# Kernel tuning notes

Hardware: AMD Instinct MI355X
Metric: run time of the kernel (lower is better)

The kernel has to match this reference:

```python
import jax, jax.numpy as jnp
import numpy as np

NCLS, NDF, B = 256, 512, 1024
ALP = 0.1


def setup_inputs() -> dict:
    key = jax.random.key(0)
    k1, k2, k3 = jax.random.split(key, 3)
    df = jax.random.normal(k1, (B, NDF), dtype=jnp.float32)
    gt = jax.random.randint(k2, (B,), 0, NCLS)
    fc = jax.random.normal(k3, (NCLS, NDF), dtype=jnp.float32)
    return {"df": df, "gt": gt, "fc": fc}


def _update_stats(df, gt):
    """Sequential per-sample running mean/var update (moving_avg=False branch).
    Faithful to the torch no_grad loop: per-class counter `it`, c1=it/(it+1),
    c2=1/(it+1); mean[t]=f when it==0 else mean[t]*c1+f*c2;
    var[t]=var[t]*c1 + (f-mean[t])**2 * c1*c2. Buffers start at zero.
    """
    mean0 = jnp.zeros((NCLS, NDF), jnp.float32)
    var0 = jnp.zeros((NCLS, NDF), jnp.float32)
    it0 = jnp.zeros((NCLS,), jnp.int32)

    def step(carry, xt):
        mean, var, it = carry
        f, t = xt
        n = it[t]
        nf = n.astype(jnp.float32)
        c1 = nf / (nf + 1.0)
        c2 = 1.0 / (nf + 1.0)
        m_t = jnp.where(n == 0, f, mean[t] * c1 + f * c2)
        a = (f - m_t) ** 2
        v_t = var[t] * c1 + a * c1 * c2
        return (mean.at[t].set(m_t), var.at[t].set(v_t), it.at[t].add(1)), None

    (mean, var, it), _ = jax.lax.scan(step, (mean0, var0, it0), (df, gt))
    return mean, var


def reference(df, gt, fc):
    # stats updated from detached features (torch uses no_grad)
    _, var = _update_stats(jax.lax.stop_gradient(df), gt)
    Var = var[gt]          # (B, ndf)
    Fc = fc[gt]            # (B, ndf): column of fc for each sample's class
    W = fc[None, :, :] - Fc[:, None, :]  # (B, ncls, ndf)
    # score[b,c] = W[b,c,:].df[b,:] + alp/2 * (W**2)[b,c,:].Var[b,:]
    score = jnp.einsum('bcd,bd->bc', W, df) \
        + 0.5 * ALP * jnp.einsum('bcd,bd->bc', W * W, Var)
    return score[:, :, None]  # (B, ncls, 1), matching torch matmul output
```

## Files before the change

### kernel.cpp

```cpp
#include <hip/hip_runtime.h>

#define NCLS 256
#define NDF  512
#define BSZ  1024
#define ALP  0.1f


typedef __attribute__((ext_vector_type(8))) short bf16x8;
typedef __attribute__((ext_vector_type(4))) float f32x4;

__device__ __forceinline__ unsigned rne_pk(float lo, float hi) {
    union { float f; unsigned u; } a, b;
    a.f = lo; b.f = hi;
    unsigned ua = (a.u + 0x7FFFu + ((a.u >> 16) & 1u)) >> 16;
    unsigned ub = (b.u + 0x7FFFu + ((b.u >> 16) & 1u)) & 0xFFFF0000u;
    return ua | ub;
}
__device__ __forceinline__ uint4 pk16(float4 p, float4 q) {
    uint4 r;
    r.x = rne_pk(p.x, p.y); r.y = rne_pk(p.z, p.w);
    r.z = rne_pk(q.x, q.y); r.w = rne_pk(q.z, q.w);
    return r;
}

__global__ __launch_bounds__(256) void fused_main(const float* __restrict__ df,
                                                  const int* __restrict__ gt,
                                                  const float* __restrict__ fc,
                                                  float* __restrict__ s1p,
                                                  float* __restrict__ Rp) {
    __shared__ union {
        struct { alignas(16) char A[64 * 256]; alignas(16) char B[64 * 256]; } g;
        struct { int gts[BSZ]; unsigned long long bmap[64 * 16]; } r;
    } sm;

    const int tid = threadIdx.x;
    const int bid = blockIdx.x;
    const int lane = tid & 63;
    const int wv = tid >> 6;
    const int wm = (wv >> 1) * 32, wn = (wv & 1) * 32;
    const int fr = lane & 15;
    const int fkb = (lane >> 4) * 16;
    const int fswz = (fr & 7) << 4;

    const int sr = tid >> 2;
    const int sswz = (sr & 7) << 4;
    char* arow = sm.g.A + sr * 256;
    char* brow = sm.g.B + sr * 256;

    f32x4 acc[2][2];
    acc[0][0] = 0.f; acc[0][1] = 0.f; acc[1][0] = 0.f; acc[1][1] = 0.f;

    auto mma_step = [&](int k0b) {
        const int kb = (k0b + fkb) ^ fswz;
        const bf16x8 aF0 = *(const bf16x8*)(sm.g.A + (wm + fr) * 256 + kb);
        const bf16x8 aF1 = *(const bf16x8*)(sm.g.A + (wm + 16 + fr) * 256 + kb);
        const bf16x8 bF0 = *(const bf16x8*)(sm.g.B + (wn + fr) * 256 + kb);
        const bf16x8 bF1 = *(const bf16x8*)(sm.g.B + (wn + 16 + fr) * 256 + kb);
        acc[0][0] = __builtin_amdgcn_mfma_f32_16x16x32_bf16(aF0, bF0, acc[0][0], 0, 0, 0);
        acc[0][1] = __builtin_amdgcn_mfma_f32_16x16x32_bf16(aF0, bF1, acc[0][1], 0, 0, 0);
        acc[1][0] = __builtin_amdgcn_mfma_f32_16x16x32_bf16(aF1, bF0, acc[1][0], 0, 0, 0);
        acc[1][1] = __builtin_amdgcn_mfma_f32_16x16x32_bf16(aF1, bF1, acc[1][1], 0, 0, 0);
    };
    auto store_tile = [&](float* base) {
#pragma unroll
        for (int mi = 0; mi < 2; ++mi)
#pragma unroll
            for (int ni = 0; ni < 2; ++ni)
#pragma unroll
                for (int r2 = 0; r2 < 4; ++r2)
                    base[(wm + mi * 16 + (lane >> 4) * 4 + r2) * NCLS + wn + ni * 16 + fr] =
                        acc[mi][ni][r2];
    };

    if (bid >= 128) {
        const int sid = bid - 128;
        const int z = sid & 3;
        const int tile = sid >> 2;
        const int bm = tile & 15, bn = tile >> 4;
        const float* Ag = df + (bm * 64 + sr) * NDF + z * 128 + (tid & 3) * 32;
        const float* Bg = fc + (bn * 64 + sr) * NDF + z * 128 + (tid & 3) * 32;
        const int kbase = (tid & 3) * 64;

        float4 a[8], b[8];
#pragma unroll
        for (int i = 0; i < 8; ++i) a[i] = ((const float4*)Ag)[i];
#pragma unroll
        for (int i = 0; i < 8; ++i) b[i] = ((const float4*)Bg)[i];
        *(uint4*)(arow + ((kbase + 0) ^ sswz)) = pk16(a[0], a[1]);
        *(uint4*)(arow + ((kbase + 16) ^ sswz)) = pk16(a[2], a[3]);
        *(uint4*)(arow + ((kbase + 32) ^ sswz)) = pk16(a[4], a[5]);
        *(uint4*)(arow + ((kbase + 48) ^ sswz)) = pk16(a[6], a[7]);
        *(uint4*)(brow + ((kbase + 0) ^ sswz)) = pk16(b[0], b[1]);
        *(uint4*)(brow + ((kbase + 16) ^ sswz)) = pk16(b[2], b[3]);
        *(uint4*)(brow + ((kbase + 32) ^ sswz)) = pk16(b[4], b[5]);
        *(uint4*)(brow + ((kbase + 48) ^ sswz)) = pk16(b[6], b[7]);
        __syncthreads();
        mma_step(0); mma_step(64); mma_step(128); mma_step(192);
        store_tile(s1p + z * (BSZ * NCLS) + (bm * 64) * NCLS + bn * 64);
    } else {
        const int z = bid & 7;
        const int tile = bid >> 3;
        const int bm = tile & 3, bn = tile >> 2;
        const int D0 = z * 64;
        const int clocal = sr;
        const int myclass = bm * 64 + clocal;
        const int dim0 = D0 + (tid & 3) * 16;
        const int kbl = (tid & 3) * 32;
        const int kbq = 128 + kbl;

        const float* Bg = fc + (bn * 64 + sr) * NDF + dim0;
        const float4 b0 = ((const float4*)Bg)[0], b1 = ((const float4*)Bg)[1],
                     b2 = ((const float4*)Bg)[2], b3 = ((const float4*)Bg)[3];

        for (int i = tid; i < BSZ; i += 256) sm.r.gts[i] = gt[i];
        for (int i = tid; i < 1024; i += 256) sm.r.bmap[i] = 0ull;
        __syncthreads();
        for (int i = tid; i < BSZ; i += 256) {
            const int c = sm.r.gts[i] - bm * 64;
            if ((unsigned)c < 64u) atomicOr(&sm.r.bmap[c * 16 + (i >> 6)], 1ull << (i & 63));
        }
        const float* fct = fc + myclass * NDF + dim0;
        float fcq[16];
        {
            const float4 q0 = ((const float4*)fct)[0], q1 = ((const float4*)fct)[1];
            const float4 q2 = ((const float4*)fct)[2], q3 = ((const float4*)fct)[3];
            fcq[0]=q0.x; fcq[1]=q0.y; fcq[2]=q0.z; fcq[3]=q0.w;
            fcq[4]=q1.x; fcq[5]=q1.y; fcq[6]=q1.z; fcq[7]=q1.w;
            fcq[8]=q2.x; fcq[9]=q2.y; fcq[10]=q2.z; fcq[11]=q2.w;
            fcq[12]=q3.x; fcq[13]=q3.y; fcq[14]=q3.z; fcq[15]=q3.w;
        }
        __syncthreads();

        float m[16], v[16];
#pragma unroll
        for (int j = 0; j < 16; ++j) { m[j] = 0.f; v[j] = 0.f; }
        float nf = 0.f;
        {
            int w = 0;
            unsigned long long bits = sm.r.bmap[clocal * 16];
            auto next = [&]() -> int {
                while (bits == 0ull) {
                    if (w >= 15) return -1;
                    bits = sm.r.bmap[clocal * 16 + (++w)];
                }
                const int b = __ffsll((unsigned long long)bits) - 1;
                bits &= bits - 1ull;
                return (w << 6) + b;
            };
            int cur = next();
            float f[16];
            if (cur >= 0) {
                const float* p = df + cur * NDF + dim0;
                const float4 q0 = ((const float4*)p)[0], q1 = ((const float4*)p)[1];
                const float4 q2 = ((const float4*)p)[2], q3 = ((const float4*)p)[3];
                f[0]=q0.x; f[1]=q0.y; f[2]=q0.z; f[3]=q0.w;
                f[4]=q1.x; f[5]=q1.y; f[6]=q1.z; f[7]=q1.w;
                f[8]=q2.x; f[9]=q2.y; f[10]=q2.z; f[11]=q2.w;
                f[12]=q3.x; f[13]=q3.y; f[14]=q3.z; f[15]=q3.w;
            }
            while (cur >= 0) {
                const int nxt = next();
                float g[16];
                if (nxt >= 0) {
                    const float* p = df + nxt * NDF + dim0;
                    const float4 q0 = ((const float4*)p)[0], q1 = ((const float4*)p)[1];
                    const float4 q2 = ((const float4*)p)[2], q3 = ((const float4*)p)[3];
                    g[0]=q0.x; g[1]=q0.y; g[2]=q0.z; g[3]=q0.w;
                    g[4]=q1.x; g[5]=q1.y; g[6]=q1.z; g[7]=q1.w;
                    g[8]=q2.x; g[9]=q2.y; g[10]=q2.z; g[11]=q2.w;
                    g[12]=q3.x; g[13]=q3.y; g[14]=q3.z; g[15]=q3.w;
                }
                const float c2 = 1.0f / (nf + 1.0f);
                const float c1 = nf * c2;
                const float c12 = c1 * c2;
#pragma unroll
                for (int j = 0; j < 16; ++j) {
                    m[j] = m[j] * c1 + f[j] * c2;
                    const float a = f[j] - m[j];
                    v[j] = v[j] * c1 + a * a * c12;
                }
                nf += 1.0f;
#pragma unroll
                for (int j = 0; j < 16; ++j) f[j] = g[j];
                cur = nxt;
            }
        }
        __syncthreads();

        {
            float4 l0, l1, l2, l3;
            l0.x=-2.f*fcq[0]*v[0];  l0.y=-2.f*fcq[1]*v[1];  l0.z=-2.f*fcq[2]*v[2];  l0.w=-2.f*fcq[3]*v[3];
            l1.x=-2.f*fcq[4]*v[4];  l1.y=-2.f*fcq[5]*v[5];  l1.z=-2.f*fcq[6]*v[6];  l1.w=-2.f*fcq[7]*v[7];
            l2.x=-2.f*fcq[8]*v[8];  l2.y=-2.f*fcq[9]*v[9];  l2.z=-2.f*fcq[10]*v[10]; l2.w=-2.f*fcq[11]*v[11];
            l3.x=-2.f*fcq[12]*v[12]; l3.y=-2.f*fcq[13]*v[13]; l3.z=-2.f*fcq[14]*v[14]; l3.w=-2.f*fcq[15]*v[15];
            float4 p0, p1, p2, p3;
            p0.x=v[0];  p0.y=v[1];  p0.z=v[2];  p0.w=v[3];
            p1.x=v[4];  p1.y=v[5];  p1.z=v[6];  p1.w=v[7];
            p2.x=v[8];  p2.y=v[9];  p2.z=v[10]; p2.w=v[11];
            p3.x=v[12]; p3.y=v[13]; p3.z=v[14]; p3.w=v[15];
            float4 s0, s1, s2, s3;
            s0.x=b0.x*b0.x; s0.y=b0.y*b0.y; s0.z=b0.z*b0.z; s0.w=b0.w*b0.w;
            s1.x=b1.x*b1.x; s1.y=b1.y*b1.y; s1.z=b1.z*b1.z; s1.w=b1.w*b1.w;
            s2.x=b2.x*b2.x; s2.y=b2.y*b2.y; s2.z=b2.z*b2.z; s2.w=b2.w*b2.w;
            s3.x=b3.x*b3.x; s3.y=b3.y*b3.y; s3.z=b3.z*b3.z; s3.w=b3.w*b3.w;
            *(uint4*)(arow + ((kbl + 0) ^ sswz)) = pk16(l0, l1);
            *(uint4*)(arow + ((kbl + 16) ^ sswz)) = pk16(l2, l3);
            *(uint4*)(arow + ((kbq + 0) ^ sswz)) = pk16(p0, p1);
            *(uint4*)(arow + ((kbq + 16) ^ sswz)) = pk16(p2, p3);
            *(uint4*)(brow + ((kbl + 0) ^ sswz)) = pk16(b0, b1);
            *(uint4*)(brow + ((kbl + 16) ^ sswz)) = pk16(b2, b3);
            *(uint4*)(brow + ((kbq + 0) ^ sswz)) = pk16(s0, s1);
            *(uint4*)(brow + ((kbq + 16) ^ sswz)) = pk16(s2, s3);
        }
        __syncthreads();
        mma_step(0); mma_step(64); mma_step(128); mma_step(192);
        store_tile(Rp + z * (NCLS * NCLS) + (bm * 64) * NCLS + bn * 64);
    }
}

__global__ __launch_bounds__(256) void epilogue_kernel(const float* __restrict__ s1p,
                                                       const float* __restrict__ Rp,
                                                       const int* __restrict__ gt,
                                                       float* __restrict__ out) {
    const int b = blockIdx.x * 4 + (threadIdx.x >> 6);
    const int cq = (threadIdx.x & 63) * 4;
    const int t = gt[b];
    float4 v1 = make_float4(0.f, 0.f, 0.f, 0.f);
    float v1t = 0.f;
#pragma unroll
    for (int zz = 0; zz < 4; ++zz) {
        const float* row = s1p + zz * (BSZ * NCLS) + b * NCLS;
        const float4 q = *(const float4*)(row + cq);
        v1.x += q.x; v1.y += q.y; v1.z += q.z; v1.w += q.w;
        v1t += row[t];
    }
    float4 vR = make_float4(0.f, 0.f, 0.f, 0.f);
    float vRt = 0.f;
#pragma unroll
    for (int zz = 0; zz < 8; ++zz) {
        const float* row = Rp + zz * (NCLS * NCLS) + t * NCLS;
        const float4 q = *(const float4*)(row + cq);
        vR.x += q.x; vR.y += q.y; vR.z += q.z; vR.w += q.w;
        vRt += row[t];
    }
    float4 o;
    o.x = (v1.x - v1t) + 0.5f * ALP * (vR.x - vRt);
    o.y = (v1.y - v1t) + 0.5f * ALP * (vR.y - vRt);
    o.z = (v1.z - v1t) + 0.5f * ALP * (vR.z - vRt);
    o.w = (v1.w - v1t) + 0.5f * ALP * (vR.w - vRt);
    *(float4*)(out + b * NCLS + cq) = o;
}

extern "C" void kernel_launch(void* const* d_in, const int* in_sizes, int n_in,
                              void* d_out, int out_size, void* d_ws, size_t ws_size,
                              hipStream_t stream) {
    const float* df = (const float*)d_in[0];
    const int* gt = (const int*)d_in[1];
    const float* fc = (const float*)d_in[2];
    float* out = (float*)d_out;

    float* ws = (float*)d_ws;
    float* s1p = ws;
    float* Rp = s1p + 4 * BSZ * NCLS;

    fused_main<<<384, 256, 0, stream>>>(df, gt, fc, s1p, Rp);
    epilogue_kernel<<<256, 256, 0, stream>>>(s1p, Rp, gt, out);
}
```

Before: 25.92 us.

## Move df·fc GEMM into epilogue kernel and precompute per-sample bias

The split-K df·fc^T GEMM that wrote four partial score slabs to workspace is removed from the first kernel. The second kernel now does the full-K GEMM on 32x32 tiles and applies the variance-term epilogue directly. The self-class term df·fc[gt] becomes a separate per-sample bias, computed by spare blocks of the first kernel with matching bf16 rounding. This drops the large s1p write and re-read in exchange for a longer K loop per block in the second kernel.

```diff
diff --git a/kernel.cpp b/kernel.cpp
--- a/kernel.cpp
+++ b/kernel.cpp
@@ -22,12 +22,17 @@
     r.z = rne_pk(q.x, q.y); r.w = rne_pk(q.z, q.w);
     return r;
 }
-
-__global__ __launch_bounds__(256) void fused_main(const float* __restrict__ df,
-                                                  const int* __restrict__ gt,
-                                                  const float* __restrict__ fc,
-                                                  float* __restrict__ s1p,
-                                                  float* __restrict__ Rp) {
+__device__ __forceinline__ float bf16r(float x) {
+    union { float f; unsigned u; } c; c.f = x;
+    c.u = (c.u + 0x7FFFu + ((c.u >> 16) & 1u)) & 0xFFFF0000u;
+    return c.f;
+}
+
+__global__ __launch_bounds__(256) void k1_R_bias(const float* __restrict__ df,
+                                                 const int* __restrict__ gt,
+                                                 const float* __restrict__ fc,
+                                                 float* __restrict__ Rp,
+                                                 float* __restrict__ bias1) {
     __shared__ union {
         struct { alignas(16) char A[64 * 256]; alignas(16) char B[64 * 256]; } g;
         struct { int gts[BSZ]; unsigned long long bmap[64 * 16]; } r;
@@ -36,6 +41,25 @@
     const int tid = threadIdx.x;
     const int bid = blockIdx.x;
     const int lane = tid & 63;
+
+    if (bid >= 128) {
+        const int b = (bid - 128) * 4 + (tid >> 6);
+        const int t = gt[b];
+        const float* pd = df + b * NDF + lane * 8;
+        const float* pf = fc + t * NDF + lane * 8;
+        const float4 d0 = ((const float4*)pd)[0], d1 = ((const float4*)pd)[1];
+        const float4 f0 = ((const float4*)pf)[0], f1 = ((const float4*)pf)[1];
+        float s = 0.f;
+        s = fmaf(bf16r(d0.x), bf16r(f0.x), s); s = fmaf(bf16r(d0.y), bf16r(f0.y), s);
+        s = fmaf(bf16r(d0.z), bf16r(f0.z), s); s = fmaf(bf16r(d0.w), bf16r(f0.w), s);
+        s = fmaf(bf16r(d1.x), bf16r(f1.x), s); s = fmaf(bf16r(d1.y), bf16r(f1.y), s);
+        s = fmaf(bf16r(d1.z), bf16r(f1.z), s); s = fmaf(bf16r(d1.w), bf16r(f1.w), s);
+#pragma unroll
+        for (int off = 32; off; off >>= 1) s += __shfl_xor(s, off, 64);
+        if (lane == 0) bias1[b] = s;
+        return;
+    }
+
     const int wv = tid >> 6;
     const int wm = (wv >> 1) * 32, wn = (wv & 1) * 32;
     const int fr = lane & 15;
@@ -61,194 +85,200 @@
         acc[1][0] = __builtin_amdgcn_mfma_f32_16x16x32_bf16(aF1, bF0, acc[1][0], 0, 0, 0);
         acc[1][1] = __builtin_amdgcn_mfma_f32_16x16x32_bf16(aF1, bF1, acc[1][1], 0, 0, 0);
     };
-    auto store_tile = [&](float* base) {
-#pragma unroll
-        for (int mi = 0; mi < 2; ++mi)
-#pragma unroll
-            for (int ni = 0; ni < 2; ++ni)
-#pragma unroll
-                for (int r2 = 0; r2 < 4; ++r2)
-                    base[(wm + mi * 16 + (lane >> 4) * 4 + r2) * NCLS + wn + ni * 16 + fr] =
-                        acc[mi][ni][r2];
-    };
-
-    if (bid >= 128) {
-        const int sid = bid - 128;
-        const int z = sid & 3;
-        const int tile = sid >> 2;
-        const int bm = tile & 15, bn = tile >> 4;
-        const float* Ag = df + (bm * 64 + sr) * NDF + z * 128 + (tid & 3) * 32;
-        const float* Bg = fc + (bn * 64 + sr) * NDF + z * 128 + (tid & 3) * 32;
-        const int kbase = (tid & 3) * 64;
-
-        float4 a[8], b[8];
-#pragma unroll
-        for (int i = 0; i < 8; ++i) a[i] = ((const float4*)Ag)[i];
-#pragma unroll
-        for (int i = 0; i < 8; ++i) b[i] = ((const float4*)Bg)[i];
-        *(uint4*)(arow + ((kbase + 0) ^ sswz)) = pk16(a[0], a[1]);
-        *(uint4*)(arow + ((kbase + 16) ^ sswz)) = pk16(a[2], a[3]);
-        *(uint4*)(arow + ((kbase + 32) ^ sswz)) = pk16(a[4], a[5]);
-        *(uint4*)(arow + ((kbase + 48) ^ sswz)) = pk16(a[6], a[7]);
-        *(uint4*)(brow + ((kbase + 0) ^ sswz)) = pk16(b[0], b[1]);
-        *(uint4*)(brow + ((kbase + 16) ^ sswz)) = pk16(b[2], b[3]);
-        *(uint4*)(brow + ((kbase + 32) ^ sswz)) = pk16(b[4], b[5]);
-        *(uint4*)(brow + ((kbase + 48) ^ sswz)) = pk16(b[6], b[7]);
-        __syncthreads();
-        mma_step(0); mma_step(64); mma_step(128); mma_step(192);
-        store_tile(s1p + z * (BSZ * NCLS) + (bm * 64) * NCLS + bn * 64);
-    } else {
-        const int z = bid & 7;
-        const int tile = bid >> 3;
-        const int bm = tile & 3, bn = tile >> 2;
-        const int D0 = z * 64;
-        const int clocal = sr;
-        const int myclass = bm * 64 + clocal;
-        const int dim0 = D0 + (tid & 3) * 16;
-        const int kbl = (tid & 3) * 32;
-        const int kbq = 128 + kbl;
-
-        const float* Bg = fc + (bn * 64 + sr) * NDF + dim0;
-        const float4 b0 = ((const float4*)Bg)[0], b1 = ((const float4*)Bg)[1],
-                     b2 = ((const float4*)Bg)[2], b3 = ((const float4*)Bg)[3];
-
-        for (int i = tid; i < BSZ; i += 256) sm.r.gts[i] = gt[i];
-        for (int i = tid; i < 1024; i += 256) sm.r.bmap[i] = 0ull;
-        __syncthreads();
-        for (int i = tid; i < BSZ; i += 256) {
-            const int c = sm.r.gts[i] - bm * 64;
-            if ((unsigned)c < 64u) atomicOr(&sm.r.bmap[c * 16 + (i >> 6)], 1ull << (i & 63));
+
+    const int z = bid & 7;
+    const int tile = bid >> 3;
+    const int bm = tile & 3, bn = tile >> 2;
+    const int D0 = z * 64;
+    const int clocal = sr;
+    const int myclass = bm * 64 + clocal;
+    const int dim0 = D0 + (tid & 3) * 16;
+    const int kbl = (tid & 3) * 32;
+    const int kbq = 128 + kbl;
+
+    const float* Bg = fc + (bn * 64 + sr) * NDF + dim0;
+    const float4 b0 = ((const float4*)Bg)[0], b1 = ((const float4*)Bg)[1],
+                 b2 = ((const float4*)Bg)[2], b3 = ((const float4*)Bg)[3];
+
+    for (int i = tid; i < BSZ; i += 256) sm.r.gts[i] = gt[i];
+    for (int i = tid; i < 1024; i += 256) sm.r.bmap[i] = 0ull;
+    __syncthreads();
+    for (int i = tid; i < BSZ; i += 256) {
+        const int c = sm.r.gts[i] - bm * 64;
+        if ((unsigned)c < 64u) atomicOr(&sm.r.bmap[c * 16 + (i >> 6)], 1ull << (i & 63));
+    }
+    const float* fct = fc + myclass * NDF + dim0;
+    float fcq[16];
+    {
+        const float4 q0 = ((const float4*)fct)[0], q1 = ((const float4*)fct)[1];
+        const float4 q2 = ((const float4*)fct)[2], q3 = ((const float4*)fct)[3];
+        fcq[0]=q0.x; fcq[1]=q0.y; fcq[2]=q0.z; fcq[3]=q0.w;
+        fcq[4]=q1.x; fcq[5]=q1.y; fcq[6]=q1.z; fcq[7]=q1.w;
+        fcq[8]=q2.x; fcq[9]=q2.y; fcq[10]=q2.z; fcq[11]=q2.w;
+        fcq[12]=q3.x; fcq[13]=q3.y; fcq[14]=q3.z; fcq[15]=q3.w;
+    }
+    __syncthreads();
+
+    float m[16], v[16];
+#pragma unroll
+    for (int j = 0; j < 16; ++j) { m[j] = 0.f; v[j] = 0.f; }
+    float nf = 0.f;
+    {
+        int w = 0;
+        unsigned long long bits = sm.r.bmap[clocal * 16];
+        auto next = [&]() -> int {
+            while (bits == 0ull) {
+                if (w >= 15) return -1;
+                bits = sm.r.bmap[clocal * 16 + (++w)];
+            }
+            const int b = __ffsll((unsigned long long)bits) - 1;
+            bits &= bits - 1ull;
+            return (w << 6) + b;
+        };
+        int cur = next();
+        float f[16];
+        if (cur >= 0) {
+            const float* p = df + cur * NDF + dim0;
+            const float4 q0 = ((const float4*)p)[0], q1 = ((const float4*)p)[1];
+            const float4 q2 = ((const float4*)p)[2], q3 = ((const float4*)p)[3];
+            f[0]=q0.x; f[1]=q0.y; f[2]=q0.z; f[3]=q0.w;
+            f[4]=q1.x; f[5]=q1.y; f[6]=q1.z; f[7]=q1.w;
+            f[8]=q2.x; f[9]=q2.y; f[10]=q2.z; f[11]=q2.w;
+            f[12]=q3.x; f[13]=q3.y; f[14]=q3.z; f[15]=q3.w;
         }
-        const float* fct = fc + myclass * NDF + dim0;
-        float fcq[16];
-        {
-            const float4 q0 = ((const float4*)fct)[0], q1 = ((const float4*)fct)[1];
-            const float4 q2 = ((const float4*)fct)[2], q3 = ((const float4*)fct)[3];
-            fcq[0]=q0.x; fcq[1]=q0.y; fcq[2]=q0.z; fcq[3]=q0.w;
-            fcq[4]=q1.x; fcq[5]=q1.y; fcq[6]=q1.z; fcq[7]=q1.w;
-            fcq[8]=q2.x; fcq[9]=q2.y; fcq[10]=q2.z; fcq[11]=q2.w;
-            fcq[12]=q3.x; fcq[13]=q3.y; fcq[14]=q3.z; fcq[15]=q3.w;
-        }
-        __syncthreads();
-
-        float m[16], v[16];
-#pragma unroll
-        for (int j = 0; j < 16; ++j) { m[j] = 0.f; v[j] = 0.f; }
-        float nf = 0.f;
-        {
-            int w = 0;
-            unsigned long long bits = sm.r.bmap[clocal * 16];
-            auto next = [&]() -> int {
-                while (bits == 0ull) {
-                    if (w >= 15) return -1;
-                    bits = sm.r.bmap[clocal * 16 + (++w)];
-                }
-                const int b = __ffsll((unsigned long long)bits) - 1;
-                bits &= bits - 1ull;
-                return (w << 6) + b;
-            };
-            int cur = next();
-            float f[16];
-            if (cur >= 0) {
-                const float* p = df + cur * NDF + dim0;
+        while (cur >= 0) {
+            const int nxt = next();
+            float g[16];
+            if (nxt >= 0) {
+                const float* p = df + nxt * NDF + dim0;
                 const float4 q0 = ((const float4*)p)[0], q1 = ((const float4*)p)[1];
                 const float4 q2 = ((const float4*)p)[2], q3 = ((const float4*)p)[3];
-                f[0]=q0.x; f[1]=q0.y; f[2]=q0.z; f[3]=q0.w;
-                f[4]=q1.x; f[5]=q1.y; f[6]=q1.z; f[7]=q1.w;
-                f[8]=q2.x; f[9]=q2.y; f[10]=q2.z; f[11]=q2.w;
-                f[12]=q3.x; f[13]=q3.y; f[14]=q3.z; f[15]=q3.w;
+                g[0]=q0.x; g[1]=q0.y; g[2]=q0.z; g[3]=q0.w;
+                g[4]=q1.x; g[5]=q1.y; g[6]=q1.z; g[7]=q1.w;
+                g[8]=q2.x; g[9]=q2.y; g[10]=q2.z; g[11]=q2.w;
+                g[12]=q3.x; g[13]=q3.y; g[14]=q3.z; g[15]=q3.w;
             }
-            while (cur >= 0) {
-                const int nxt = next();
-                float g[16];
-                if (nxt >= 0) {
-                    const float* p = df + nxt * NDF + dim0;
-                    const float4 q0 = ((const float4*)p)[0], q1 = ((const float4*)p)[1];
-                    const float4 q2 = ((const float4*)p)[2], q3 = ((const float4*)p)[3];
-                    g[0]=q0.x; g[1]=q0.y; g[2]=q0.z; g[3]=q0.w;
-                    g[4]=q1.x; g[5]=q1.y; g[6]=q1.z; g[7]=q1.w;
-                    g[8]=q2.x; g[9]=q2.y; g[10]=q2.z; g[11]=q2.w;
-                    g[12]=q3.x; g[13]=q3.y; g[14]=q3.z; g[15]=q3.w;
-                }
-                const float c2 = 1.0f / (nf + 1.0f);
-                const float c1 = nf * c2;
-                const float c12 = c1 * c2;
-#pragma unroll
-                for (int j = 0; j < 16; ++j) {
-                    m[j] = m[j] * c1 + f[j] * c2;
-                    const float a = f[j] - m[j];
-                    v[j] = v[j] * c1 + a * a * c12;
-                }
-                nf += 1.0f;
-#pragma unroll
-                for (int j = 0; j < 16; ++j) f[j] = g[j];
-                cur = nxt;
+            const float c2 = 1.0f / (nf + 1.0f);
+            const float c1 = nf * c2;
+            const float c12 = c1 * c2;
+#pragma unroll
+            for (int j = 0; j < 16; ++j) {
+                m[j] = m[j] * c1 + f[j] * c2;
+                const float a = f[j] - m[j];
+                v[j] = v[j] * c1 + a * a * c12;
             }
+            nf += 1.0f;
+#pragma unroll
+            for (int j = 0; j < 16; ++j) f[j] = g[j];
+            cur = nxt;
         }
-        __syncthreads();
-
-        {
-            float4 l0, l1, l2, l3;
-            l0.x=-2.f*fcq[0]*v[0];  l0.y=-2.f*fcq[1]*v[1];  l0.z=-2.f*fcq[2]*v[2];  l0.w=-2.f*fcq[3]*v[3];
-            l1.x=-2.f*fcq[4]*v[4];  l1.y=-2.f*fcq[5]*v[5];  l1.z=-2.f*fcq[6]*v[6];  l1.w=-2.f*fcq[7]*v[7];
-            l2.x=-2.f*fcq[8]*v[8];  l2.y=-2.f*fcq[9]*v[9];  l2.z=-2.f*fcq[10]*v[10]; l2.w=-2.f*fcq[11]*v[11];
-            l3.x=-2.f*fcq[12]*v[12]; l3.y=-2.f*fcq[13]*v[13]; l3.z=-2.f*fcq[14]*v[14]; l3.w=-2.f*fcq[15]*v[15];
-            float4 p0, p1, p2, p3;
-            p0.x=v[0];  p0.y=v[1];  p0.z=v[2];  p0.w=v[3];
-            p1.x=v[4];  p1.y=v[5];  p1.z=v[6];  p1.w=v[7];
-            p2.x=v[8];  p2.y=v[9];  p2.z=v[10]; p2.w=v[11];
-            p3.x=v[12]; p3.y=v[13]; p3.z=v[14]; p3.w=v[15];
-            float4 s0, s1, s2, s3;
-            s0.x=b0.x*b0.x; s0.y=b0.y*b0.y; s0.z=b0.z*b0.z; s0.w=b0.w*b0.w;
-            s1.x=b1.x*b1.x; s1.y=b1.y*b1.y; s1.z=b1.z*b1.z; s1.w=b1.w*b1.w;
-            s2.x=b2.x*b2.x; s2.y=b2.y*b2.y; s2.z=b2.z*b2.z; s2.w=b2.w*b2.w;
-            s3.x=b3.x*b3.x; s3.y=b3.y*b3.y; s3.z=b3.z*b3.z; s3.w=b3.w*b3.w;
-            *(uint4*)(arow + ((kbl + 0) ^ sswz)) = pk16(l0, l1);
-            *(uint4*)(arow + ((kbl + 16) ^ sswz)) = pk16(l2, l3);
-            *(uint4*)(arow + ((kbq + 0) ^ sswz)) = pk16(p0, p1);
-            *(uint4*)(arow + ((kbq + 16) ^ sswz)) = pk16(p2, p3);
-            *(uint4*)(brow + ((kbl + 0) ^ sswz)) = pk16(b0, b1);
-            *(uint4*)(brow + ((kbl + 16) ^ sswz)) = pk16(b2, b3);
-            *(uint4*)(brow + ((kbq + 0) ^ sswz)) = pk16(s0, s1);
-            *(uint4*)(brow + ((kbq + 16) ^ sswz)) = pk16(s2, s3);
+    }
+    __syncthreads();
+
+    {
+        float4 l0, l1, l2, l3;
+        l0.x=-2.f*fcq[0]*v[0];  l0.y=-2.f*fcq[1]*v[1];  l0.z=-2.f*fcq[2]*v[2];  l0.w=-2.f*fcq[3]*v[3];
+        l1.x=-2.f*fcq[4]*v[4];  l1.y=-2.f*fcq[5]*v[5];  l1.z=-2.f*fcq[6]*v[6];  l1.w=-2.f*fcq[7]*v[7];
+        l2.x=-2.f*fcq[8]*v[8];  l2.y=-2.f*fcq[9]*v[9];  l2.z=-2.f*fcq[10]*v[10]; l2.w=-2.f*fcq[11]*v[11];
+        l3.x=-2.f*fcq[12]*v[12]; l3.y=-2.f*fcq[13]*v[13]; l3.z=-2.f*fcq[14]*v[14]; l3.w=-2.f*fcq[15]*v[15];
+        float4 p0, p1, p2, p3;
+        p0.x=v[0];  p0.y=v[1];  p0.z=v[2];  p0.w=v[3];
+        p1.x=v[4];  p1.y=v[5];  p1.z=v[6];  p1.w=v[7];
+        p2.x=v[8];  p2.y=v[9];  p2.z=v[10]; p2.w=v[11];
+        p3.x=v[12]; p3.y=v[13]; p3.z=v[14]; p3.w=v[15];
+        float4 s0, s1, s2, s3;
+        s0.x=b0.x*b0.x; s0.y=b0.y*b0.y; s0.z=b0.z*b0.z; s0.w=b0.w*b0.w;
+        s1.x=b1.x*b1.x; s1.y=b1.y*b1.y; s1.z=b1.z*b1.z; s1.w=b1.w*b1.w;
+        s2.x=b2.x*b2.x; s2.y=b2.y*b2.y; s2.z=b2.z*b2.z; s2.w=b2.w*b2.w;
+        s3.x=b3.x*b3.x; s3.y=b3.y*b3.y; s3.z=b3.z*b3.z; s3.w=b3.w*b3.w;
+        *(uint4*)(arow + ((kbl + 0) ^ sswz)) = pk16(l0, l1);
+        *(uint4*)(arow + ((kbl + 16) ^ sswz)) = pk16(l2, l3);
+        *(uint4*)(arow + ((kbq + 0) ^ sswz)) = pk16(p0, p1);
+        *(uint4*)(arow + ((kbq + 16) ^ sswz)) = pk16(p2, p3);
+        *(uint4*)(brow + ((kbl + 0) ^ sswz)) = pk16(b0, b1);
+        *(uint4*)(brow + ((kbl + 16) ^ sswz)) = pk16(b2, b3);
+        *(uint4*)(brow + ((kbq + 0) ^ sswz)) = pk16(s0, s1);
+        *(uint4*)(brow + ((kbq + 16) ^ sswz)) = pk16(s2, s3);
+    }
+    __syncthreads();
+    mma_step(0); mma_step(64); mma_step(128); mma_step(192);
+
+    float* base = Rp + z * (NCLS * NCLS) + (bm * 64) * NCLS + bn * 64;
+#pragma unroll
+    for (int mi = 0; mi < 2; ++mi)
+#pragma unroll
+        for (int ni = 0; ni < 2; ++ni)
+#pragma unroll
+            for (int r2 = 0; r2 < 4; ++r2)
+                base[(wm + mi * 16 + (lane >> 4) * 4 + r2) * NCLS + wn + ni * 16 + fr] =
+                    acc[mi][ni][r2];
+}
+
+__global__ __launch_bounds__(256, 2) void k2_s1_out(const float* __restrict__ df,
+                                                    const int* __restrict__ gt,
+                                                    const float* __restrict__ fc,
+                                                    const float* __restrict__ Rp,
+                                                    const float* __restrict__ bias1,
+                                                    float* __restrict__ out) {
+    __shared__ alignas(16) char A[32 * 1024];
+    __shared__ alignas(16) char B[32 * 1024];
+
+    const int tid = threadIdx.x;
+    const int bn = blockIdx.x & 7, bm = blockIdx.x >> 3;
+
+    const int row = tid >> 3, kc = tid & 7;
+    const float* Ag = df + (bm * 32 + row) * NDF + kc * 64;
+    const float* Bg = fc + (bn * 32 + row) * NDF + kc * 64;
+    float4 a[16], b[16];
+#pragma unroll
+    for (int i = 0; i < 16; ++i) a[i] = ((const float4*)Ag)[i];
+#pragma unroll
+    for (int i = 0; i < 16; ++i) b[i] = ((const float4*)Bg)[i];
+    const int swz = (row & 7) << 4;
+    char* ar = A + row * 1024;
+    char* br = B + row * 1024;
+#pragma unroll
+    for (int i = 0; i < 8; ++i)
+        *(uint4*)(ar + ((kc * 128 + i * 16) ^ swz)) = pk16(a[2 * i], a[2 * i + 1]);
+#pragma unroll
+    for (int i = 0; i < 8; ++i)
+        *(uint4*)(br + ((kc * 128 + i * 16) ^ swz)) = pk16(b[2 * i], b[2 * i + 1]);
+    __syncthreads();
+
+    const int lane = tid & 63;
+    const int wv = tid >> 6;
+    const int wm = (wv >> 1) * 16, wn = (wv & 1) * 16;
+    const int fr = lane & 15;
+    const int fkb = (lane >> 4) * 16;
+    const int fswz = (fr & 7) << 4;
+    f32x4 accE = 0.f, accO = 0.f;
+#pragma unroll
+    for (int s = 0; s < 16; s += 2) {
+        const int kb0 = (s * 64 + fkb) ^ fswz;
+        const int kb1 = ((s + 1) * 64 + fkb) ^ fswz;
+        const bf16x8 aF0 = *(const bf16x8*)(A + (wm + fr) * 1024 + kb0);
+        const bf16x8 bF0 = *(const bf16x8*)(B + (wn + fr) * 1024 + kb0);
+        const bf16x8 aF1 = *(const bf16x8*)(A + (wm + fr) * 1024 + kb1);
+        const bf16x8 bF1 = *(const bf16x8*)(B + (wn + fr) * 1024 + kb1);
+        accE = __builtin_amdgcn_mfma_f32_16x16x32_bf16(aF0, bF0, accE, 0, 0, 0);
+        accO = __builtin_amdgcn_mfma_f32_16x16x32_bf16(aF1, bF1, accO, 0, 0, 0);
+    }
+
+    const int colg = bn * 32 + wn + fr;
+#pragma unroll
+    for (int r = 0; r < 4; ++r) {
+        const int bg = bm * 32 + wm + (lane >> 4) * 4 + r;
+        const int t = gt[bg];
+        float vR = 0.f, vtt = 0.f;
+#pragma unroll
+        for (int z = 0; z < 8; ++z) {
+            const float* rp = Rp + z * (NCLS * NCLS) + t * NCLS;
+            vR += rp[colg];
+            vtt += rp[t];
         }
-        __syncthreads();
-        mma_step(0); mma_step(64); mma_step(128); mma_step(192);
-        store_tile(Rp + z * (NCLS * NCLS) + (bm * 64) * NCLS + bn * 64);
-    }
-}
-
-__global__ __launch_bounds__(256) void epilogue_kernel(const float* __restrict__ s1p,
-                                                       const float* __restrict__ Rp,
-                                                       const int* __restrict__ gt,
-                                                       float* __restrict__ out) {
-    const int b = blockIdx.x * 4 + (threadIdx.x >> 6);
-    const int cq = (threadIdx.x & 63) * 4;
-    const int t = gt[b];
-    float4 v1 = make_float4(0.f, 0.f, 0.f, 0.f);
-    float v1t = 0.f;
-#pragma unroll
-    for (int zz = 0; zz < 4; ++zz) {
-        const float* row = s1p + zz * (BSZ * NCLS) + b * NCLS;
-        const float4 q = *(const float4*)(row + cq);
-        v1.x += q.x; v1.y += q.y; v1.z += q.z; v1.w += q.w;
-        v1t += row[t];
-    }
-    float4 vR = make_float4(0.f, 0.f, 0.f, 0.f);
-    float vRt = 0.f;
-#pragma unroll
-    for (int zz = 0; zz < 8; ++zz) {
-        const float* row = Rp + zz * (NCLS * NCLS) + t * NCLS;
-        const float4 q = *(const float4*)(row + cq);
-        vR.x += q.x; vR.y += q.y; vR.z += q.z; vR.w += q.w;
-        vRt += row[t];
-    }
-    float4 o;
-    o.x = (v1.x - v1t) + 0.5f * ALP * (vR.x - vRt);
-    o.y = (v1.y - v1t) + 0.5f * ALP * (vR.y - vRt);
-    o.z = (v1.z - v1t) + 0.5f * ALP * (vR.z - vRt);
-    o.w = (v1.w - v1t) + 0.5f * ALP * (vR.w - vRt);
-    *(float4*)(out + b * NCLS + cq) = o;
+        const float v1 = accE[r] + accO[r] - bias1[bg];
+        out[bg * NCLS + colg] = v1 + 0.5f * ALP * (vR - vtt);
+    }
 }
 
 extern "C" void kernel_launch(void* const* d_in, const int* in_sizes, int n_in,
@@ -260,9 +290,9 @@
     float* out = (float*)d_out;
 
     float* ws = (float*)d_ws;
-    float* s1p = ws;
-    float* Rp = s1p + 4 * BSZ * NCLS;
-
-    fused_main<<<384, 256, 0, stream>>>(df, gt, fc, s1p, Rp);
-    epilogue_kernel<<<256, 256, 0, stream>>>(s1p, Rp, gt, out);
-}
+    float* Rp = ws;
+    float* bias1 = Rp + 8 * NCLS * NCLS;
+
+    k1_R_bias<<<384, 256, 0, stream>>>(df, gt, fc, Rp, bias1);
+    k2_s1_out<<<256, 256, 0, stream>>>(df, gt, fc, Rp, bias1, out);
+}
```

New measurement: 24.95 us (median of 2 runs). -3.7%, faster.
